# Optimization experiments

Measured on AMD Instinct MI355X. Metric: run time of the kernel, lower is better.

## Reference

```python
import jax, jax.numpy as jnp
import numpy as np

B, C, H, W, L = 2, 64, 48, 48, 48
GH, GW, GL = 24, 24, 24  # gating signal at half resolution


def setup_inputs() -> dict:
    key = jax.random.key(0)
    k = jax.random.split(key, 6)
    x = jax.random.normal(k[0], (B, C, H, W, L), dtype=jnp.float32)
    g = jax.random.normal(k[1], (B, C, GH, GW, GL), dtype=jnp.float32)
    s = 1.0 / np.sqrt(C)
    W1 = jax.random.normal(k[2], (C, C), dtype=jnp.float32) * s  # conv1 1x1x1 weight (out,in)
    b1 = jax.random.normal(k[3], (C,), dtype=jnp.float32) * 0.01
    W2 = jax.random.normal(k[4], (C, C), dtype=jnp.float32) * s  # conv2 1x1x1 weight
    b2 = jax.random.normal(k[5], (C,), dtype=jnp.float32) * 0.01
    return {"x": x, "g": g, "W1": W1, "b1": b1, "W2": W2, "b2": b2}


def _conv1x1(v, Wm, b):
    # 1x1x1 Conv3d == channel-mixing matmul
    return jnp.einsum('bchwl,oc->bohwl', v, Wm) + b[None, :, None, None, None]


def reference(x, g, W1, b1, W2, b2):
    theta_x = _conv1x1(x, W1, b1)                       # (B, C, H, W, L)
    theta_g = _conv1x1(g, W2, b2)                       # (B, C, GH, GW, GL)
    # F.upsample(mode='trilinear', align_corners=False) -> half-pixel trilinear resize
    theta_g = jax.image.resize(theta_g, (B, C, H, W, L), method='trilinear')

    # spatially-normalized elementwise gate
    theta_c = theta_x * theta_g
    theta_c = theta_c - jnp.min(theta_c)                # global min over whole tensor
    theta_c = theta_c / jnp.sum(theta_c, axis=(2, 3, 4), keepdims=True)
    p = theta_c * x

    # channel-channel attention per (b,h,w), contracting over L
    theta_c_d = jnp.einsum('bihwl,bjhwl->bhwij', theta_x, theta_g)  # (B,H,W,C,C)
    theta_c_d = theta_c_d - jnp.min(theta_c_d)
    theta_c_d = theta_c_d / jnp.sum(theta_c_d, axis=(1, 2, 3, 4), keepdims=True)
    d = jnp.einsum('bchwl,bhwcj->bjhwl', x, theta_c_d)  # (B, C, H, W, L)
    return (p, d)
```

## Files before the change

### kernel.cpp

```cpp
#include <hip/hip_runtime.h>

#define Bb 2
#define Cc 64
#define Hh 48
#define Ww 48
#define Ll 48
#define HWc (Hh*Ww)
#define HWL (HWc*Ll)
#define GHh 24
#define SG (GHh*GHh*GHh)
#define NBLK (Bb*HWc)
#define CNT1f 110592.0f
#define CNT2f 9437184.0f

__device__ __forceinline__ void interp1(int i, int& a, int& b, float& f){
  float src = i*0.5f - 0.25f;
  float fl = floorf(src);
  f = src - fl;
  int i0 = (int)fl;
  a = i0 < 0 ? 0 : i0;
  int i1 = i0 + 1;
  b = i1 > (GHh-1) ? (GHh-1) : i1;
}

__global__ __launch_bounds__(256) void conv_k(const float* __restrict__ in,
    const float* __restrict__ Wm, const float* __restrict__ bias,
    float* __restrict__ out, int S){
  __shared__ __align__(16) float Wl[64][68];
  __shared__ __align__(16) float xl[64][68];
  int t = threadIdx.x;
  int ntile = S >> 6;
  int b  = blockIdx.x / ntile;
  int s0 = (blockIdx.x % ntile) << 6;
  for (int q = t; q < 4096; q += 256){
    int o = q >> 6, c = q & 63;
    Wl[c][o] = Wm[q];
  }
  const float* inb = in + (size_t)b*Cc*S + s0;
  for (int q = t; q < 1024; q += 256){
    int c = q >> 4, v = (q & 15) << 2;
    float4 val = *(const float4*)(inb + (size_t)c*S + v);
    *(float4*)&xl[c][v] = val;
  }
  __syncthreads();
  int o0 = (t & 15) << 2, s1 = (t >> 4) << 2;
  float a00=0,a01=0,a02=0,a03=0,a10=0,a11=0,a12=0,a13=0;
  float a20=0,a21=0,a22=0,a23=0,a30=0,a31=0,a32=0,a33=0;
  #pragma unroll 8
  for (int c = 0; c < 64; ++c){
    float4 wv = *(const float4*)&Wl[c][o0];
    float4 xv = *(const float4*)&xl[c][s1];
    a00 += wv.x*xv.x; a01 += wv.x*xv.y; a02 += wv.x*xv.z; a03 += wv.x*xv.w;
    a10 += wv.y*xv.x; a11 += wv.y*xv.y; a12 += wv.y*xv.z; a13 += wv.y*xv.w;
    a20 += wv.z*xv.x; a21 += wv.z*xv.y; a22 += wv.z*xv.z; a23 += wv.z*xv.w;
    a30 += wv.w*xv.x; a31 += wv.w*xv.y; a32 += wv.w*xv.z; a33 += wv.w*xv.w;
  }
  float* ob = out + (size_t)b*Cc*S + s0 + s1;
  float b0 = bias[o0+0], b1v = bias[o0+1], b2v = bias[o0+2], b3 = bias[o0+3];
  { float4 r = make_float4(a00+b0,a01+b0,a02+b0,a03+b0); *(float4*)(ob + (size_t)(o0+0)*S) = r; }
  { float4 r = make_float4(a10+b1v,a11+b1v,a12+b1v,a13+b1v); *(float4*)(ob + (size_t)(o0+1)*S) = r; }
  { float4 r = make_float4(a20+b2v,a21+b2v,a22+b2v,a23+b2v); *(float4*)(ob + (size_t)(o0+2)*S) = r; }
  { float4 r = make_float4(a30+b3,a31+b3,a32+b3,a33+b3); *(float4*)(ob + (size_t)(o0+3)*S) = r; }
}

__device__ __forceinline__ void g_fold(const float* __restrict__ txt,
    float* __restrict__ G, int t){
  int c = t >> 2, kb = (t & 3)*6;
  const float* T = &txt[c*52];
  #pragma unroll
  for (int i = 0; i < 6; ++i){
    int k = kb + i;
    float v;
    if (k == 0)       v = T[0] + 0.75f*T[1] + 0.25f*T[2];
    else if (k == 23) v = 0.25f*T[45] + 0.75f*T[46] + T[47];
    else              v = 0.25f*T[2*k-1] + 0.75f*T[2*k]
                        + 0.75f*T[2*k+1] + 0.25f*T[2*k+2];
    G[k*68 + c] = v;
  }
}

__global__ __launch_bounds__(256) void reduce_k(const float* __restrict__ tx,
    const float* __restrict__ tgh, float* __restrict__ msite,
    float* __restrict__ part_row, float* __restrict__ pm1,
    float* __restrict__ pm2, float* __restrict__ ps2){
  __shared__ __align__(16) float sh[7224];
  float* txt = sh;
  float* M   = sh + 3328;
  float* G   = sh + 4960;
  float* red = sh + 6592;
  float* sxg = sh + 7104;
  float* CM  = sh + 7152;
  float* SX  = sh + 7176;
  int t = threadIdx.x;
  int bIdx = blockIdx.x;
  int b = bIdx / HWc, hw = bIdx % HWc;
  int h = hw / Ww, w = hw % Ww;
  int ha, hb; float fh; interp1(h, ha, hb, fh);
  int wa, wb; float fw; interp1(w, wa, wb, fw);
  float omh = 1.f - fh, omw = 1.f - fw;
  const float* txb = tx + ((size_t)b*Cc*HWc + hw)*Ll;
  #pragma unroll
  for (int k = 0; k < 3; ++k){
    int q = t + (k << 8);
    int c = q / 12, v = (q % 12) << 2;
    *(float4*)&txt[c*52+v] = *(const float4*)(txb + (size_t)c*HWL + v);
  }
  const float* gb = tgh + (size_t)b*Cc*SG;
  for (int u = t; u < 384; u += 256){
    int c = u / 6, s4 = (u % 6) << 2;
    const float* gc = gb + (size_t)c*SG;
    float4 vaa = *(const float4*)(gc + ha*576 + wa*24 + s4);
    float4 vba = *(const float4*)(gc + hb*576 + wa*24 + s4);
    float4 vab = *(const float4*)(gc + ha*576 + wb*24 + s4);
    float4 vbb = *(const float4*)(gc + hb*576 + wb*24 + s4);
    M[(s4+0)*68 + c] = omw*(omh*vaa.x + fh*vba.x) + fw*(omh*vab.x + fh*vbb.x);
    M[(s4+1)*68 + c] = omw*(omh*vaa.y + fh*vba.y) + fw*(omh*vab.y + fh*vbb.y);
    M[(s4+2)*68 + c] = omw*(omh*vaa.z + fh*vba.z) + fw*(omh*vab.z + fh*vbb.z);
    M[(s4+3)*68 + c] = omw*(omh*vaa.w + fh*vba.w) + fw*(omh*vab.w + fh*vbb.w);
  }
  __syncthreads();
  g_fold(txt, G, t);
  if (t < 24){
    float s = 0.f;
    #pragma unroll 8
    for (int c = 0; c < 64; ++c) s += M[t*68 + c];
    CM[t] = s;
  }
  if (t >= 192 && t < 240){
    int l = t - 192;
    float s = 0.f;
    #pragma unroll 8
    for (int c = 0; c < 64; ++c) s += txt[c*52 + l];
    SX[l] = s;
  }
  __syncthreads();
  int c = t & 63, lg = t >> 6;
  float psum = 0.f, pmin = 3.4e38f;
  const float* Trow = &txt[c*52];
  #pragma unroll
  for (int li = 0; li < 12; ++li){
    int l = lg*12 + li;
    int la, lb; float fl; interp1(l, la, lb, fl);
    float tgv = (1.f-fl)*M[la*68 + c] + fl*M[lb*68 + c];
    float prod = Trow[l]*tgv;
    psum += prod;
    pmin = fminf(pmin, prod);
  }
  red[t] = psum;
  if (t < 48){
    int la, lb; float fl; interp1(t, la, lb, fl);
    sxg[t] = SX[t] * ((1.f-fl)*CM[la] + fl*CM[lb]);
  }
  float* msb = msite + (size_t)bIdx*1536;
  for (int u = t; u < 384; u += 256){
    int k = u >> 4, c4 = (u & 15) << 2;
    float4 mv;
    mv.x = M[k*68+c4+0]; mv.y = M[k*68+c4+1];
    mv.z = M[k*68+c4+2]; mv.w = M[k*68+c4+3];
    *(float4*)(msb + (u << 2)) = mv;
  }
  int i0 = (t & 15) << 2, j0 = (t >> 4) << 2;
  float a00=0,a01=0,a02=0,a03=0,a10=0,a11=0,a12=0,a13=0;
  float a20=0,a21=0,a22=0,a23=0,a30=0,a31=0,a32=0,a33=0;
  #pragma unroll 4
  for (int k = 0; k < 24; ++k){
    float4 gv = *(const float4*)&G[k*68 + i0];
    float4 mv = *(const float4*)&M[k*68 + j0];
    a00 += gv.x*mv.x; a01 += gv.x*mv.y; a02 += gv.x*mv.z; a03 += gv.x*mv.w;
    a10 += gv.y*mv.x; a11 += gv.y*mv.y; a12 += gv.y*mv.z; a13 += gv.y*mv.w;
    a20 += gv.z*mv.x; a21 += gv.z*mv.y; a22 += gv.z*mv.z; a23 += gv.z*mv.w;
    a30 += gv.w*mv.x; a31 += gv.w*mv.y; a32 += gv.w*mv.z; a33 += gv.w*mv.w;
  }
  float amin = fminf(fminf(fminf(a00,a01),fminf(a02,a03)),
               fminf(fminf(fminf(a10,a11),fminf(a12,a13)),
               fminf(fminf(fminf(a20,a21),fminf(a22,a23)),
                     fminf(fminf(a30,a31),fminf(a32,a33)))));
  __syncthreads();
  if (t < 64) part_row[(size_t)bIdx*64 + t] = red[t]+red[t+64]+red[t+128]+red[t+192];
  __syncthreads();
  red[t] = pmin; red[256+t] = amin;
  __syncthreads();
  if (t < 128){
    red[t] = fminf(red[t], red[t+128]);
    red[256+t] = fminf(red[256+t], red[384+t]);
  }
  __syncthreads();
  if (t < 64){
    float v1 = fminf(red[t], red[t+64]);
    float v2 = fminf(red[256+t], red[320+t]);
    #pragma unroll
    for (int off = 32; off; off >>= 1){
      v1 = fminf(v1, __shfl_down(v1, off));
      v2 = fminf(v2, __shfl_down(v2, off));
    }
    if (t == 0){
      pm1[bIdx] = v1; pm2[bIdx] = v2;
      float tot = 0.f;
      #pragma unroll
      for (int l = 0; l < 48; ++l) tot += sxg[l];
      ps2[bIdx] = tot;
    }
  }
}

__global__ __launch_bounds__(256) void reduce2_k(const float* __restrict__ part_row,
    const float* __restrict__ pm1, const float* __restrict__ pm2,
    const float* __restrict__ ps2, float* __restrict__ rowsum,
    float* __restrict__ gmin, float* __restrict__ s2v){
  __shared__ float red[512];
  int t = threadIdx.x, blk = blockIdx.x;
  if (blk < 128){
    int b = blk >> 6, c = blk & 63;
    const float* src = part_row + (size_t)b*HWc*64 + c;
    float s = 0.f;
    #pragma unroll
    for (int k = 0; k < 9; ++k){
      int i = t + (k << 8);
      s += src[(size_t)i*64];
    }
    red[t] = s; __syncthreads();
    for (int sgap = 128; sgap >= 64; sgap >>= 1){
      if (t < sgap) red[t] += red[t+sgap];
      __syncthreads();
    }
    if (t < 64){
      float v = red[t];
      #pragma unroll
      for (int off = 32; off; off >>= 1) v += __shfl_down(v, off);
      if (t == 0) rowsum[blk] = v;
    }
  } else if (blk == 128){
    float m1 = 3.4e38f, m2 = 3.4e38f;
    for (int i = t; i < NBLK; i += 256){ m1 = fminf(m1, pm1[i]); m2 = fminf(m2, pm2[i]); }
    red[t] = m1; red[256+t] = m2; __syncthreads();
    for (int s = 128; s >= 1; s >>= 1){
      if (t < s){ red[t] = fminf(red[t], red[t+s]); red[256+t] = fminf(red[256+t], red[256+t+s]); }
      __syncthreads();
    }
    if (t == 0){ gmin[0] = red[0]; gmin[1] = red[256]; }
  } else {
    float sa = 0.f, sb = 0.f;
    for (int i = t; i < HWc; i += 256){ sa += ps2[i]; sb += ps2[HWc + i]; }
    red[t] = sa; red[256+t] = sb; __syncthreads();
    for (int s = 128; s >= 1; s >>= 1){
      if (t < s){ red[t] += red[t+s]; red[256+t] += red[256+t+s]; }
      __syncthreads();
    }
    if (t == 0){ s2v[0] = red[0]; s2v[1] = red[256]; }
  }
}

__global__ __launch_bounds__(256) void final_k(const float* __restrict__ x,
    const float* __restrict__ tx, const float* __restrict__ msite,
    const float* __restrict__ gmin, const float* __restrict__ rowsum,
    const float* __restrict__ s2v, float* __restrict__ outp, float* __restrict__ outd){
  __shared__ __align__(16) float sh[9984];
  float* txt = sh;
  float* xs  = sh + 3328;
  float* M   = sh + 6656;
  float* G   = sh + 8288;
  float* iv1 = sh + 9920;
  int t = threadIdx.x;
  int bIdx = blockIdx.x;
  int b = bIdx / HWc, hw = bIdx % HWc;
  size_t sbase = ((size_t)b*Cc*HWc + hw)*Ll;
  const float* txb = tx + sbase;
  const float* xb  = x  + sbase;
  float m1 = gmin[0], m2 = gmin[1];
  #pragma unroll
  for (int k = 0; k < 3; ++k){
    int q = t + (k << 8);
    int c = q / 12, v = (q % 12) << 2;
    *(float4*)&txt[c*52+v] = *(const float4*)(txb + (size_t)c*HWL + v);
    *(float4*)&xs [c*52+v] = *(const float4*)(xb  + (size_t)c*HWL + v);
  }
  const float* msb = msite + (size_t)bIdx*1536;
  for (int u = t; u < 384; u += 256){
    float4 mv = *(const float4*)(msb + (u << 2));
    int k = u >> 4, c4 = (u & 15) << 2;
    *(float4*)&M[k*68 + c4] = mv;
  }
  if (t < 64) iv1[t] = 1.f/(rowsum[b*64 + t] - m1*CNT1f);
  float invd2 = 1.f/(s2v[b] - m2*CNT2f);
  __syncthreads();
  g_fold(txt, G, t);
  __syncthreads();
  int i0 = (t & 15) << 2, j0 = (t >> 4) << 2;
  float a00=0,a01=0,a02=0,a03=0,a10=0,a11=0,a12=0,a13=0;
  float a20=0,a21=0,a22=0,a23=0,a30=0,a31=0,a32=0,a33=0;
  #pragma unroll 4
  for (int k = 0; k < 24; ++k){
    float4 gv = *(const float4*)&G[k*68 + i0];
    float4 mv = *(const float4*)&M[k*68 + j0];
    a00 += gv.x*mv.x; a01 += gv.x*mv.y; a02 += gv.x*mv.z; a03 += gv.x*mv.w;
    a10 += gv.y*mv.x; a11 += gv.y*mv.y; a12 += gv.y*mv.z; a13 += gv.y*mv.w;
    a20 += gv.z*mv.x; a21 += gv.z*mv.y; a22 += gv.z*mv.z; a23 += gv.z*mv.w;
    a30 += gv.w*mv.x; a31 += gv.w*mv.y; a32 += gv.w*mv.z; a33 += gv.w*mv.w;
  }
  #pragma unroll
  for (int k = 0; k < 3; ++k){
    int q = t + (k << 8);
    int c = q / 12, l4 = (q % 12) << 2;
    float4 a  = *(const float4*)&txt[c*52+l4];
    float4 xv = *(const float4*)&xs [c*52+l4];
    float s = iv1[c];
    float4 r;
    {
      int la, lb; float fl; interp1(l4+0, la, lb, fl);
      float tgv = (1.f-fl)*M[la*68+c] + fl*M[lb*68+c];
      r.x = (a.x*tgv - m1)*s*xv.x;
    }
    {
      int la, lb; float fl; interp1(l4+1, la, lb, fl);
      float tgv = (1.f-fl)*M[la*68+c] + fl*M[lb*68+c];
      r.y = (a.y*tgv - m1)*s*xv.y;
    }
    {
      int la, lb; float fl; interp1(l4+2, la, lb, fl);
      float tgv = (1.f-fl)*M[la*68+c] + fl*M[lb*68+c];
      r.z = (a.z*tgv - m1)*s*xv.z;
    }
    {
      int la, lb; float fl; interp1(l4+3, la, lb, fl);
      float tgv = (1.f-fl)*M[la*68+c] + fl*M[lb*68+c];
      r.w = (a.w*tgv - m1)*s*xv.w;
    }
    *(float4*)(outp + sbase + (size_t)c*HWL + l4) = r;
  }
  __syncthreads();
  float* At = txt;
  { float4 r = make_float4((a00-m2)*invd2,(a01-m2)*invd2,(a02-m2)*invd2,(a03-m2)*invd2);
    *(float4*)&At[(i0+0)*52 + j0] = r; }
  { float4 r = make_float4((a10-m2)*invd2,(a11-m2)*invd2,(a12-m2)*invd2,(a13-m2)*invd2);
    *(float4*)&At[(i0+1)*52 + j0] = r; }
  { float4 r = make_float4((a20-m2)*invd2,(a21-m2)*invd2,(a22-m2)*invd2,(a23-m2)*invd2);
    *(float4*)&At[(i0+2)*52 + j0] = r; }
  { float4 r = make_float4((a30-m2)*invd2,(a31-m2)*invd2,(a32-m2)*invd2,(a33-m2)*invd2);
    *(float4*)&At[(i0+3)*52 + j0] = r; }
  __syncthreads();
  if (t < 192){
    int jj = (t & 15) << 2, l0 = (t >> 4) << 2;
    float d00=0,d01=0,d02=0,d03=0,d10=0,d11=0,d12=0,d13=0;
    float d20=0,d21=0,d22=0,d23=0,d30=0,d31=0,d32=0,d33=0;
    #pragma unroll 4
    for (int cc = 0; cc < 64; ++cc){
      float4 av = *(const float4*)&At[cc*52 + jj];
      float4 xv = *(const float4*)&xs[cc*52 + l0];
      d00 += av.x*xv.x; d01 += av.x*xv.y; d02 += av.x*xv.z; d03 += av.x*xv.w;
      d10 += av.y*xv.x; d11 += av.y*xv.y; d12 += av.y*xv.z; d13 += av.y*xv.w;
      d20 += av.z*xv.x; d21 += av.z*xv.y; d22 += av.z*xv.z; d23 += av.z*xv.w;
      d30 += av.w*xv.x; d31 += av.w*xv.y; d32 += av.w*xv.z; d33 += av.w*xv.w;
    }
    { float4 r = make_float4(d00,d01,d02,d03);
      *(float4*)(outd + sbase + (size_t)(jj+0)*HWL + l0) = r; }
    { float4 r = make_float4(d10,d11,d12,d13);
      *(float4*)(outd + sbase + (size_t)(jj+1)*HWL + l0) = r; }
    { float4 r = make_float4(d20,d21,d22,d23);
      *(float4*)(outd + sbase + (size_t)(jj+2)*HWL + l0) = r; }
    { float4 r = make_float4(d30,d31,d32,d33);
      *(float4*)(outd + sbase + (size_t)(jj+3)*HWL + l0) = r; }
  }
}

extern "C" void kernel_launch(void* const* d_in, const int* in_sizes, int n_in,
                              void* d_out, int out_size, void* d_ws, size_t ws_size,
                              hipStream_t stream){
  (void)in_sizes; (void)n_in; (void)out_size; (void)ws_size;
  const float* x  = (const float*)d_in[0];
  const float* g  = (const float*)d_in[1];
  const float* W1 = (const float*)d_in[2];
  const float* b1 = (const float*)d_in[3];
  const float* W2 = (const float*)d_in[4];
  const float* b2 = (const float*)d_in[5];
  float* outp = (float*)d_out;
  float* outd = outp + (size_t)Bb*Cc*HWL;
  float* ws   = (float*)d_ws;
  float* txw    = ws;
  float* tghw   = txw + (size_t)Bb*Cc*HWL;
  float* msite  = tghw + (size_t)Bb*Cc*SG;
  float* part_row = msite + (size_t)NBLK*1536;
  float* pm1 = part_row + (size_t)NBLK*64;
  float* pm2 = pm1 + NBLK;
  float* ps2 = pm2 + NBLK;
  float* rowsum = ps2 + NBLK;
  float* gmin = rowsum + 128;
  float* s2v  = gmin + 2;

  hipLaunchKernelGGL(conv_k, dim3(Bb*(SG/64)), dim3(256), 0, stream, g, W2, b2, tghw, SG);
  hipLaunchKernelGGL(conv_k, dim3(Bb*(HWL/64)), dim3(256), 0, stream, x, W1, b1, txw, HWL);
  hipLaunchKernelGGL(reduce_k, dim3(NBLK), dim3(256), 0, stream, txw, tghw, msite,
                     part_row, pm1, pm2, ps2);
  hipLaunchKernelGGL(reduce2_k, dim3(130), dim3(256), 0, stream, part_row, pm1, pm2, ps2,
                     rowsum, gmin, s2v);
  hipLaunchKernelGGL(final_k, dim3(NBLK), dim3(256), 0, stream, x, txw, msite,
                     gmin, rowsum, s2v, outp, outd);
}
```

Before: 306.3 us.

## Refactor channel attention into two small GEMMs and regather gate in final kernel

The final kernel no longer builds the 64x64 channel-attention matrix. It computes P = G·x (24x48) and then d = Mᵀ·P, applying the min shift through a per-l channel sum of x, which cuts the FLOPs spent on the d output. The msite workspace buffer is removed: final_k recomputes the trilinear-gathered gate M from tgh instead of reading it back. The row sums for p are taken from the diagonal of the G·M product rather than from a separate sum over the elementwise product. In exchange there is extra gather work, scalar non-vectorised stores for d, and a slightly different floating-point summation order.

```diff
diff --git a/kernel.cpp b/kernel.cpp
--- a/kernel.cpp
+++ b/kernel.cpp
@@ -79,33 +79,10 @@
   }
 }
 
-__global__ __launch_bounds__(256) void reduce_k(const float* __restrict__ tx,
-    const float* __restrict__ tgh, float* __restrict__ msite,
-    float* __restrict__ part_row, float* __restrict__ pm1,
-    float* __restrict__ pm2, float* __restrict__ ps2){
-  __shared__ __align__(16) float sh[7224];
-  float* txt = sh;
-  float* M   = sh + 3328;
-  float* G   = sh + 4960;
-  float* red = sh + 6592;
-  float* sxg = sh + 7104;
-  float* CM  = sh + 7152;
-  float* SX  = sh + 7176;
-  int t = threadIdx.x;
-  int bIdx = blockIdx.x;
-  int b = bIdx / HWc, hw = bIdx % HWc;
-  int h = hw / Ww, w = hw % Ww;
-  int ha, hb; float fh; interp1(h, ha, hb, fh);
-  int wa, wb; float fw; interp1(w, wa, wb, fw);
+__device__ __forceinline__ void gather_m(const float* __restrict__ gb,
+    float* __restrict__ M, int t, int ha, int hb, int wa, int wb,
+    float fh, float fw){
   float omh = 1.f - fh, omw = 1.f - fw;
-  const float* txb = tx + ((size_t)b*Cc*HWc + hw)*Ll;
-  #pragma unroll
-  for (int k = 0; k < 3; ++k){
-    int q = t + (k << 8);
-    int c = q / 12, v = (q % 12) << 2;
-    *(float4*)&txt[c*52+v] = *(const float4*)(txb + (size_t)c*HWL + v);
-  }
-  const float* gb = tgh + (size_t)b*Cc*SG;
   for (int u = t; u < 384; u += 256){
     int c = u / 6, s4 = (u % 6) << 2;
     const float* gc = gb + (size_t)c*SG;
@@ -118,6 +95,33 @@
     M[(s4+2)*68 + c] = omw*(omh*vaa.z + fh*vba.z) + fw*(omh*vab.z + fh*vbb.z);
     M[(s4+3)*68 + c] = omw*(omh*vaa.w + fh*vba.w) + fw*(omh*vab.w + fh*vbb.w);
   }
+}
+
+__global__ __launch_bounds__(256) void reduce_k(const float* __restrict__ tx,
+    const float* __restrict__ tgh, float* __restrict__ part_row,
+    float* __restrict__ pm1, float* __restrict__ pm2, float* __restrict__ ps2){
+  __shared__ __align__(16) float sh[7224];
+  float* txt = sh;
+  float* M   = sh + 3328;
+  float* G   = sh + 4960;
+  float* red = sh + 6592;
+  float* CM  = sh + 7104;
+  float* SX  = sh + 7128;
+  float* sxg = sh + 7176;
+  int t = threadIdx.x;
+  int bIdx = blockIdx.x;
+  int b = bIdx / HWc, hw = bIdx % HWc;
+  int h = hw / Ww, w = hw % Ww;
+  int ha, hb; float fh; interp1(h, ha, hb, fh);
+  int wa, wb; float fw; interp1(w, wa, wb, fw);
+  const float* txb = tx + ((size_t)b*Cc*HWc + hw)*Ll;
+  #pragma unroll
+  for (int k = 0; k < 3; ++k){
+    int q = t + (k << 8);
+    int c = q / 12, v = (q % 12) << 2;
+    *(float4*)&txt[c*52+v] = *(const float4*)(txb + (size_t)c*HWL + v);
+  }
+  gather_m(tgh + (size_t)b*Cc*SG, M, t, ha, hb, wa, wb, fh, fw);
   __syncthreads();
   g_fold(txt, G, t);
   if (t < 24){
@@ -135,29 +139,18 @@
   }
   __syncthreads();
   int c = t & 63, lg = t >> 6;
-  float psum = 0.f, pmin = 3.4e38f;
+  float pmin = 3.4e38f;
   const float* Trow = &txt[c*52];
   #pragma unroll
   for (int li = 0; li < 12; ++li){
     int l = lg*12 + li;
     int la, lb; float fl; interp1(l, la, lb, fl);
     float tgv = (1.f-fl)*M[la*68 + c] + fl*M[lb*68 + c];
-    float prod = Trow[l]*tgv;
-    psum += prod;
-    pmin = fminf(pmin, prod);
-  }
-  red[t] = psum;
+    pmin = fminf(pmin, Trow[l]*tgv);
+  }
   if (t < 48){
     int la, lb; float fl; interp1(t, la, lb, fl);
     sxg[t] = SX[t] * ((1.f-fl)*CM[la] + fl*CM[lb]);
-  }
-  float* msb = msite + (size_t)bIdx*1536;
-  for (int u = t; u < 384; u += 256){
-    int k = u >> 4, c4 = (u & 15) << 2;
-    float4 mv;
-    mv.x = M[k*68+c4+0]; mv.y = M[k*68+c4+1];
-    mv.z = M[k*68+c4+2]; mv.w = M[k*68+c4+3];
-    *(float4*)(msb + (u << 2)) = mv;
   }
   int i0 = (t & 15) << 2, j0 = (t >> 4) << 2;
   float a00=0,a01=0,a02=0,a03=0,a10=0,a11=0,a12=0,a13=0;
@@ -175,9 +168,10 @@
                fminf(fminf(fminf(a10,a11),fminf(a12,a13)),
                fminf(fminf(fminf(a20,a21),fminf(a22,a23)),
                      fminf(fminf(a30,a31),fminf(a32,a33)))));
-  __syncthreads();
-  if (t < 64) part_row[(size_t)bIdx*64 + t] = red[t]+red[t+64]+red[t+128]+red[t+192];
-  __syncthreads();
+  if ((t & 15) == (t >> 4)){
+    float* pr = part_row + (size_t)bIdx*64 + i0;
+    pr[0] = a00; pr[1] = a11; pr[2] = a22; pr[3] = a33;
+  }
   red[t] = pmin; red[256+t] = amin;
   __syncthreads();
   if (t < 128){
@@ -251,18 +245,22 @@
 }
 
 __global__ __launch_bounds__(256) void final_k(const float* __restrict__ x,
-    const float* __restrict__ tx, const float* __restrict__ msite,
+    const float* __restrict__ tx, const float* __restrict__ tgh,
     const float* __restrict__ gmin, const float* __restrict__ rowsum,
     const float* __restrict__ s2v, float* __restrict__ outp, float* __restrict__ outd){
-  __shared__ __align__(16) float sh[9984];
+  __shared__ __align__(16) float sh[10032];
   float* txt = sh;
   float* xs  = sh + 3328;
   float* M   = sh + 6656;
   float* G   = sh + 8288;
   float* iv1 = sh + 9920;
+  float* Xs  = sh + 9984;
   int t = threadIdx.x;
   int bIdx = blockIdx.x;
   int b = bIdx / HWc, hw = bIdx % HWc;
+  int h = hw / Ww, w = hw % Ww;
+  int ha, hb; float fh; interp1(h, ha, hb, fh);
+  int wa, wb; float fw; interp1(w, wa, wb, fw);
   size_t sbase = ((size_t)b*Cc*HWc + hw)*Ll;
   const float* txb = tx + sbase;
   const float* xb  = x  + sbase;
@@ -274,29 +272,19 @@
     *(float4*)&txt[c*52+v] = *(const float4*)(txb + (size_t)c*HWL + v);
     *(float4*)&xs [c*52+v] = *(const float4*)(xb  + (size_t)c*HWL + v);
   }
-  const float* msb = msite + (size_t)bIdx*1536;
-  for (int u = t; u < 384; u += 256){
-    float4 mv = *(const float4*)(msb + (u << 2));
-    int k = u >> 4, c4 = (u & 15) << 2;
-    *(float4*)&M[k*68 + c4] = mv;
-  }
+  gather_m(tgh + (size_t)b*Cc*SG, M, t, ha, hb, wa, wb, fh, fw);
+  __syncthreads();
+  g_fold(txt, G, t);
   if (t < 64) iv1[t] = 1.f/(rowsum[b*64 + t] - m1*CNT1f);
+  if (t >= 192 && t < 240){
+    int l = t - 192;
+    float s = 0.f;
+    #pragma unroll 8
+    for (int c = 0; c < 64; ++c) s += xs[c*52 + l];
+    Xs[l] = s;
+  }
   float invd2 = 1.f/(s2v[b] - m2*CNT2f);
   __syncthreads();
-  g_fold(txt, G, t);
-  __syncthreads();
-  int i0 = (t & 15) << 2, j0 = (t >> 4) << 2;
-  float a00=0,a01=0,a02=0,a03=0,a10=0,a11=0,a12=0,a13=0;
-  float a20=0,a21=0,a22=0,a23=0,a30=0,a31=0,a32=0,a33=0;
-  #pragma unroll 4
-  for (int k = 0; k < 24; ++k){
-    float4 gv = *(const float4*)&G[k*68 + i0];
-    float4 mv = *(const float4*)&M[k*68 + j0];
-    a00 += gv.x*mv.x; a01 += gv.x*mv.y; a02 += gv.x*mv.z; a03 += gv.x*mv.w;
-    a10 += gv.y*mv.x; a11 += gv.y*mv.y; a12 += gv.y*mv.z; a13 += gv.y*mv.w;
-    a20 += gv.z*mv.x; a21 += gv.z*mv.y; a22 += gv.z*mv.z; a23 += gv.z*mv.w;
-    a30 += gv.w*mv.x; a31 += gv.w*mv.y; a32 += gv.w*mv.z; a33 += gv.w*mv.w;
-  }
   #pragma unroll
   for (int k = 0; k < 3; ++k){
     int q = t + (k << 8);
@@ -328,37 +316,45 @@
     *(float4*)(outp + sbase + (size_t)c*HWL + l4) = r;
   }
   __syncthreads();
-  float* At = txt;
-  { float4 r = make_float4((a00-m2)*invd2,(a01-m2)*invd2,(a02-m2)*invd2,(a03-m2)*invd2);
-    *(float4*)&At[(i0+0)*52 + j0] = r; }
-  { float4 r = make_float4((a10-m2)*invd2,(a11-m2)*invd2,(a12-m2)*invd2,(a13-m2)*invd2);
-    *(float4*)&At[(i0+1)*52 + j0] = r; }
-  { float4 r = make_float4((a20-m2)*invd2,(a21-m2)*invd2,(a22-m2)*invd2,(a23-m2)*invd2);
-    *(float4*)&At[(i0+2)*52 + j0] = r; }
-  { float4 r = make_float4((a30-m2)*invd2,(a31-m2)*invd2,(a32-m2)*invd2,(a33-m2)*invd2);
-    *(float4*)&At[(i0+3)*52 + j0] = r; }
-  __syncthreads();
+  float* P = txt;
   if (t < 192){
-    int jj = (t & 15) << 2, l0 = (t >> 4) << 2;
-    float d00=0,d01=0,d02=0,d03=0,d10=0,d11=0,d12=0,d13=0;
-    float d20=0,d21=0,d22=0,d23=0,d30=0,d31=0,d32=0,d33=0;
+    int k0 = t >> 3, l0 = (t & 7)*6;
+    float c0=0,c1=0,c2=0,c3=0,c4=0,c5=0;
+    const float* Gr = &G[k0*68];
+    #pragma unroll 8
+    for (int i = 0; i < 64; ++i){
+      float gv = Gr[i];
+      const float* xr = &xs[i*52 + l0];
+      c0 += gv*xr[0]; c1 += gv*xr[1]; c2 += gv*xr[2];
+      c3 += gv*xr[3]; c4 += gv*xr[4]; c5 += gv*xr[5];
+    }
+    float* pr = &P[k0*52 + l0];
+    pr[0]=c0; pr[1]=c1; pr[2]=c2; pr[3]=c3; pr[4]=c4; pr[5]=c5;
+  }
+  __syncthreads();
+  {
+    int j0 = (t >> 4) << 2, l0 = (t & 15)*3;
+    float d00=0,d01=0,d02=0,d10=0,d11=0,d12=0;
+    float d20=0,d21=0,d22=0,d30=0,d31=0,d32=0;
     #pragma unroll 4
-    for (int cc = 0; cc < 64; ++cc){
-      float4 av = *(const float4*)&At[cc*52 + jj];
-      float4 xv = *(const float4*)&xs[cc*52 + l0];
-      d00 += av.x*xv.x; d01 += av.x*xv.y; d02 += av.x*xv.z; d03 += av.x*xv.w;
-      d10 += av.y*xv.x; d11 += av.y*xv.y; d12 += av.y*xv.z; d13 += av.y*xv.w;
-      d20 += av.z*xv.x; d21 += av.z*xv.y; d22 += av.z*xv.z; d23 += av.z*xv.w;
-      d30 += av.w*xv.x; d31 += av.w*xv.y; d32 += av.w*xv.z; d33 += av.w*xv.w;
-    }
-    { float4 r = make_float4(d00,d01,d02,d03);
-      *(float4*)(outd + sbase + (size_t)(jj+0)*HWL + l0) = r; }
-    { float4 r = make_float4(d10,d11,d12,d13);
-      *(float4*)(outd + sbase + (size_t)(jj+1)*HWL + l0) = r; }
-    { float4 r = make_float4(d20,d21,d22,d23);
-      *(float4*)(outd + sbase + (size_t)(jj+2)*HWL + l0) = r; }
-    { float4 r = make_float4(d30,d31,d32,d33);
-      *(float4*)(outd + sbase + (size_t)(jj+3)*HWL + l0) = r; }
+    for (int k = 0; k < 24; ++k){
+      float4 mv = *(const float4*)&M[k*68 + j0];
+      const float* pr = &P[k*52 + l0];
+      float p0 = pr[0], p1 = pr[1], p2 = pr[2];
+      d00 += mv.x*p0; d01 += mv.x*p1; d02 += mv.x*p2;
+      d10 += mv.y*p0; d11 += mv.y*p1; d12 += mv.y*p2;
+      d20 += mv.z*p0; d21 += mv.z*p1; d22 += mv.z*p2;
+      d30 += mv.w*p0; d31 += mv.w*p1; d32 += mv.w*p2;
+    }
+    float x0 = m2*Xs[l0+0], x1 = m2*Xs[l0+1], x2 = m2*Xs[l0+2];
+    float* o0 = outd + sbase + (size_t)(j0+0)*HWL + l0;
+    float* o1 = outd + sbase + (size_t)(j0+1)*HWL + l0;
+    float* o2 = outd + sbase + (size_t)(j0+2)*HWL + l0;
+    float* o3 = outd + sbase + (size_t)(j0+3)*HWL + l0;
+    o0[0]=(d00-x0)*invd2; o0[1]=(d01-x1)*invd2; o0[2]=(d02-x2)*invd2;
+    o1[0]=(d10-x0)*invd2; o1[1]=(d11-x1)*invd2; o1[2]=(d12-x2)*invd2;
+    o2[0]=(d20-x0)*invd2; o2[1]=(d21-x1)*invd2; o2[2]=(d22-x2)*invd2;
+    o3[0]=(d30-x0)*invd2; o3[1]=(d31-x1)*invd2; o3[2]=(d32-x2)*invd2;
   }
 }
 
@@ -377,8 +373,7 @@
   float* ws   = (float*)d_ws;
   float* txw    = ws;
   float* tghw   = txw + (size_t)Bb*Cc*HWL;
-  float* msite  = tghw + (size_t)Bb*Cc*SG;
-  float* part_row = msite + (size_t)NBLK*1536;
+  float* part_row = tghw + (size_t)Bb*Cc*SG;
   float* pm1 = part_row + (size_t)NBLK*64;
   float* pm2 = pm1 + NBLK;
   float* ps2 = pm2 + NBLK;
@@ -388,10 +383,10 @@
 
   hipLaunchKernelGGL(conv_k, dim3(Bb*(SG/64)), dim3(256), 0, stream, g, W2, b2, tghw, SG);
   hipLaunchKernelGGL(conv_k, dim3(Bb*(HWL/64)), dim3(256), 0, stream, x, W1, b1, txw, HWL);
-  hipLaunchKernelGGL(reduce_k, dim3(NBLK), dim3(256), 0, stream, txw, tghw, msite,
+  hipLaunchKernelGGL(reduce_k, dim3(NBLK), dim3(256), 0, stream, txw, tghw,
                      part_row, pm1, pm2, ps2);
   hipLaunchKernelGGL(reduce2_k, dim3(130), dim3(256), 0, stream, part_row, pm1, pm2, ps2,
                      rowsum, gmin, s2v);
-  hipLaunchKernelGGL(final_k, dim3(NBLK), dim3(256), 0, stream, x, txw, msite,
+  hipLaunchKernelGGL(final_k, dim3(NBLK), dim3(256), 0, stream, x, txw, tghw,
                      gmin, rowsum, s2v, outp, outd);
 }
```

New measurement: 310.7 us. No clear change (+1.4%).
